# Optimization experiments

Hardware: AMD Instinct MI355X
Metric: run time of the kernel (lower is better)

The kernel has to match this reference:

```python
import jax, jax.numpy as jnp
import numpy as np

N = 50000
E = 600000
IN_DIM = 256
H1, H2, H3 = 128, 64, 64
HEADS = 8


def _add_self_loops(edge_index, edge_weight=None):
    loop = jnp.arange(N, dtype=edge_index.dtype)
    src = jnp.concatenate([edge_index[0], loop])
    dst = jnp.concatenate([edge_index[1], loop])
    if edge_weight is None:
        return src, dst, None
    ew = jnp.concatenate([edge_weight, jnp.ones((N,), edge_weight.dtype)])
    return src, dst, ew


def gcn_conv(x, edge_index, edge_weight, W, b):
    # PyG GCNConv: add self-loops (weight 1), symmetric normalization, scatter-add.
    src, dst, ew = _add_self_loops(edge_index, edge_weight)
    deg = jax.ops.segment_sum(ew, dst, num_segments=N)          # [N]
    dinv = jnp.where(deg > 0, jax.lax.rsqrt(jnp.maximum(deg, 1e-12)), 0.0)
    coeff = dinv[src] * ew * dinv[dst]                          # [E+N]
    h = x @ W                                                    # [N, out]
    out = jax.ops.segment_sum(coeff[:, None] * h[src], dst, num_segments=N)
    return out + b


def gat_conv(x, edge_index, W, att_src, att_dst, b):
    # PyG GATConv, heads=HEADS, concat=False (mean over heads), leaky_relu slope 0.2.
    src, dst, _ = _add_self_loops(edge_index)
    C = W.shape[1] // HEADS
    h = (x @ W).reshape(N, HEADS, C)                             # [N,H,C]
    a_s = jnp.sum(h * att_src, axis=-1)                          # [N,H]
    a_d = jnp.sum(h * att_dst, axis=-1)                          # [N,H]
    e = jax.nn.leaky_relu(a_s[src] + a_d[dst], negative_slope=0.2)  # [E',H]
    # scatter-softmax over edges sharing a destination
    m = jax.ops.segment_max(e, dst, num_segments=N)              # [N,H]
    p = jnp.exp(e - m[dst])
    s = jax.ops.segment_sum(p, dst, num_segments=N)              # [N,H]
    alpha = p / (s[dst] + 1e-16)                                 # [E',H]
    out = jax.ops.segment_sum(alpha[:, :, None] * h[src], dst, num_segments=N)  # [N,H,C]
    return jnp.mean(out, axis=1) + b


def setup_inputs() -> dict:
    key = jax.random.key(0)
    ks = jax.random.split(key, 12)
    x = jax.random.normal(ks[0], (N, IN_DIM), dtype=jnp.float32)
    edge_index = jax.random.randint(ks[1], (2, E), 0, N, dtype=jnp.int32)
    edge_weight = jax.random.uniform(ks[2], (E,), dtype=jnp.float32)
    def glorot(k, shape):
        fan = shape[0] + shape[-1]
        return jax.random.normal(k, shape, dtype=jnp.float32) * np.sqrt(2.0 / fan)
    return {
        "x": x, "edge_index": edge_index, "edge_weight": edge_weight,
        "gc1_w": glorot(ks[3], (IN_DIM, H1)), "gc1_b": jnp.zeros((H1,), jnp.float32),
        "gat_w": glorot(ks[4], (H1, HEADS * H2)),
        "att_src": glorot(ks[5], (HEADS, H2)), "att_dst": glorot(ks[6], (HEADS, H2)),
        "gat_b": jnp.zeros((H2,), jnp.float32),
        "gc2_w": glorot(ks[7], (H2, H3)), "gc2_b": jnp.zeros((H3,), jnp.float32),
        "fc_w": glorot(ks[8], (H3, 1)), "fc_b": jnp.zeros((1,), jnp.float32),
    }


def reference(x, edge_index, edge_weight, gc1_w, gc1_b, gat_w, att_src, att_dst,
              gat_b, gc2_w, gc2_b, fc_w, fc_b):
    # dropout is inference no-op
    h = jax.nn.relu(gcn_conv(x, edge_index, edge_weight, gc1_w, gc1_b))
    h = jax.nn.relu(gat_conv(h, edge_index, gat_w, att_src, att_dst, gat_b))
    h = jax.nn.relu(gcn_conv(h, edge_index, edge_weight, gc2_w, gc2_b))
    return h @ fc_w + fc_b                                       # [N,1]
```

## Files before the change

### kernel.cpp

```cpp
#include <hip/hip_runtime.h>
#include <hip/hip_bf16.h>

#define GNN_N 50000
#define GNN_E 600000

typedef unsigned int uint;
typedef unsigned short ushort;
using short8 = __attribute__((ext_vector_type(8))) short;
using f32x4  = __attribute__((ext_vector_type(4))) float;

__device__ __forceinline__ float leaky02(float x) { return x > 0.f ? x : 0.2f * x; }
__device__ __forceinline__ ushort f2b(float f) {
    uint u = __float_as_uint(f);
    return (ushort)((u + 0x7fffu + ((u >> 16) & 1u)) >> 16);
}
__device__ __forceinline__ float b2f(ushort b) { return __uint_as_float(((uint)b) << 16); }
__device__ __forceinline__ float blo(uint u) { return __uint_as_float(u << 16); }
__device__ __forceinline__ float bhi(uint u) { return __uint_as_float(u & 0xffff0000u); }

__global__ void gnn_hist(const int* __restrict__ dst, int* __restrict__ cnt, int e) {
    int i = blockIdx.x * blockDim.x + threadIdx.x;
    if (i < e) atomicAdd(&cnt[dst[i]], 1);
}
__global__ void gnn_scan1(const int* __restrict__ cnt, int* __restrict__ row_ptr,
                          int* __restrict__ blksum, int n) {
    __shared__ int sh[256];
    int tid = threadIdx.x;
    int base = blockIdx.x * 1024 + tid * 4;
    int v0 = (base + 0 < n) ? cnt[base + 0] : 0;
    int v1 = (base + 1 < n) ? cnt[base + 1] : 0;
    int v2 = (base + 2 < n) ? cnt[base + 2] : 0;
    int v3 = (base + 3 < n) ? cnt[base + 3] : 0;
    int tsum = v0 + v1 + v2 + v3;
    sh[tid] = tsum;
    __syncthreads();
    for (int off = 1; off < 256; off <<= 1) {
        int t = (tid >= off) ? sh[tid - off] : 0;
        __syncthreads();
        sh[tid] += t;
        __syncthreads();
    }
    int excl = sh[tid] - tsum;
    if (base + 0 < n) row_ptr[base + 0] = excl; excl += v0;
    if (base + 1 < n) row_ptr[base + 1] = excl; excl += v1;
    if (base + 2 < n) row_ptr[base + 2] = excl; excl += v2;
    if (base + 3 < n) row_ptr[base + 3] = excl;
    if (tid == 255) blksum[blockIdx.x] = sh[255];
}
__global__ void gnn_scan2(int* blksum, int nblk, int* row_ptr_end, int total) {
    if (threadIdx.x == 0 && blockIdx.x == 0) {
        int run = 0;
        for (int b = 0; b < nblk; ++b) { int t = blksum[b]; blksum[b] = run; run += t; }
        *row_ptr_end = total;
    }
}
__global__ void gnn_scan3(int* row_ptr, const int* __restrict__ blksum, int n) {
    int i = blockIdx.x * blockDim.x + threadIdx.x;
    if (i < n) row_ptr[i] += blksum[i >> 10];
}
__global__ void gnn_scatter_idx(const int* __restrict__ dst, const int* __restrict__ row_ptr,
                                int* __restrict__ fill, int* __restrict__ tord, int e) {
    int i = blockIdx.x * blockDim.x + threadIdx.x;
    if (i >= e) return;
    int d = dst[i];
    int pos = row_ptr[d] + atomicAdd(&fill[d], 1);
    tord[pos] = i;
}
__global__ void gnn_sortdeg(const float* __restrict__ ew, int* __restrict__ tord,
                            const int* __restrict__ row_ptr, float* __restrict__ dinv, int n) {
    int v = blockIdx.x * blockDim.x + threadIdx.x;
    if (v >= n) return;
    int beg = row_ptr[v], end = row_ptr[v + 1];
    int d = end - beg;
    if (d <= 64) {
        int buf[64];
        for (int i = 0; i < d; ++i) buf[i] = tord[beg + i];
        for (int i = 1; i < d; ++i) {
            int key = buf[i];
            int k = i - 1;
            while (k >= 0 && buf[k] > key) { buf[k + 1] = buf[k]; --k; }
            buf[k + 1] = key;
        }
        float s = 1.f;
        for (int i = 0; i < d; ++i) { tord[beg + i] = buf[i]; s += ew[buf[i]]; }
        dinv[v] = rsqrtf(s);
    } else {
        for (int i = beg + 1; i < end; ++i) {
            int key = tord[i];
            int k = i - 1;
            while (k >= beg && tord[k] > key) { tord[k + 1] = tord[k]; --k; }
            tord[k + 1] = key;
        }
        float s = 1.f;
        for (int i = beg; i < end; ++i) s += ew[tord[i]];
        dinv[v] = rsqrtf(s);
    }
}
__global__ void gnn_edgefin(const int* __restrict__ src, const int* __restrict__ dst,
                            const float* __restrict__ ew, const float* __restrict__ dinv,
                            const int* __restrict__ tord, int* __restrict__ esrc,
                            float* __restrict__ ecw, int e) {
    int pos = blockIdx.x * blockDim.x + threadIdx.x;
    if (pos >= e) return;
    int i = tord[pos];
    int s = src[i];
    esrc[pos] = s;
    ecw[pos] = dinv[s] * ew[i] * dinv[dst[i]];
}

__global__ void gnn_prep(const float* __restrict__ gc1_w, const float* __restrict__ gat_w,
                         const float* __restrict__ gc2_w, const float* __restrict__ att_src,
                         const float* __restrict__ att_dst, ushort* __restrict__ w1t,
                         ushort* __restrict__ w2s_t, ushort* __restrict__ w3t,
                         float* __restrict__ wa_t) {
    int t = blockIdx.x * 256 + threadIdx.x;
    if (t < 32768) {
        int k = t >> 7, n = t & 127;
        w1t[n * 256 + k] = f2b(gc1_w[t]);
        return;
    }
    t -= 32768;
    if (t < 65536) {
        int c = t >> 10, r = t & 1023;
        int h = r >> 7, k = r & 127;
        w2s_t[t] = f2b(0.125f * gat_w[(size_t)k * 512 + h * 64 + c]);
        return;
    }
    t -= 65536;
    if (t < 4096) {
        int k = t >> 6, n = t & 63;
        w3t[n * 64 + k] = f2b(gc2_w[t]);
        return;
    }
    t -= 4096;
    if (t < 2048) {
        int j = t >> 7, k = t & 127;
        int h = j & 7;
        const float* av = (j < 8) ? att_src : att_dst;
        float s = 0.f;
        for (int c = 0; c < 64; ++c) s += gat_w[(size_t)k * 512 + h * 64 + c] * av[h * 64 + c];
        wa_t[j * 128 + k] = s;
    }
}

template <bool AF32, bool BIAS>
__global__ __launch_bounds__(256) void gnn_mfma_gemm(const void* __restrict__ Av,
                                                     const ushort* __restrict__ Bt,
                                                     ushort* __restrict__ C,
                                                     const float* __restrict__ bias,
                                                     int M, int N, int K) {
    __shared__ ushort As[64 * 40];
    __shared__ ushort Bs[64 * 40];
    const int tid = threadIdx.x;
    const int wv = tid >> 6, lane = tid & 63;
    const int g = lane >> 4, r = lane & 15;
    const int brow = blockIdx.y << 6, bcol = blockIdx.x << 6;

    const int srow = tid >> 2;
    const int skoff = (tid & 3) << 3;
    int arow = brow + srow;
    if (arow >= M) arow = M - 1;
    const ushort* A16 = (const ushort*)Av;
    const float*  A32 = (const float*)Av;
    const ushort* Ap16 = A16 + (size_t)arow * K + skoff;
    const float*  Ap32 = A32 + (size_t)arow * K + skoff;
    const ushort* Bp = Bt + (size_t)(bcol + srow) * K + skoff;
    ushort* AsW = &As[srow * 40 + skoff];
    ushort* BsW = &Bs[srow * 40 + skoff];

    f32x4 acc[4] = {};

    for (int k0 = 0; k0 < K; k0 += 32) {
        if constexpr (AF32) {
            float4 f0 = *(const float4*)(Ap32 + k0);
            float4 f1 = *(const float4*)(Ap32 + k0 + 4);
            short8 t;
            t[0] = (short)f2b(f0.x); t[1] = (short)f2b(f0.y);
            t[2] = (short)f2b(f0.z); t[3] = (short)f2b(f0.w);
            t[4] = (short)f2b(f1.x); t[5] = (short)f2b(f1.y);
            t[6] = (short)f2b(f1.z); t[7] = (short)f2b(f1.w);
            *(short8*)AsW = t;
        } else {
            *(short8*)AsW = *(const short8*)(Ap16 + k0);
        }
        *(short8*)BsW = *(const short8*)(Bp + k0);
        __syncthreads();
        short8 bfrag = *(const short8*)&Bs[(wv * 16 + r) * 40 + g * 8];
#pragma unroll
        for (int mb = 0; mb < 4; ++mb) {
            short8 afrag = *(const short8*)&As[(mb * 16 + r) * 40 + g * 8];
            acc[mb] = __builtin_amdgcn_mfma_f32_16x16x32_bf16(afrag, bfrag, acc[mb], 0, 0, 0);
        }
        __syncthreads();
    }

    const int col = bcol + wv * 16 + r;
    float bv = 0.f;
    if constexpr (BIAS) bv = bias[col];
#pragma unroll
    for (int mb = 0; mb < 4; ++mb) {
        int rowb = brow + mb * 16 + g * 4;
#pragma unroll
        for (int rr = 0; rr < 4; ++rr) {
            int row = rowb + rr;
            if (row < M) {
                float val = acc[mb][rr];
                if constexpr (BIAS) {
                    val += bv;
                    val = val > 0.f ? val : 0.f;
                }
                C[(size_t)row * N + col] = f2b(val);
            }
        }
    }
}

__global__ __launch_bounds__(256) void gnn_gcn_node128_asd(const int* __restrict__ row_ptr,
                                                           const int* __restrict__ esrc,
                                                           const float* __restrict__ ecw,
                                                           const float* __restrict__ dinv,
                                                           const ushort* __restrict__ hb,
                                                           const float* __restrict__ b,
                                                           const float* __restrict__ wa,
                                                           ushort* __restrict__ out,
                                                           float* __restrict__ a_s,
                                                           float* __restrict__ a_d, int n) {
    __shared__ float swa[16 * 128];
    for (int i = threadIdx.x; i < 16 * 128; i += 256) swa[i] = wa[i];
    __syncthreads();
    int v = blockIdx.x * 4 + (threadIdx.x >> 6);
    int lane = threadIdx.x & 63;
    if (v >= n) return;
    const int sl = lane & 31;
    const int half = lane >> 5;
    float di = dinv[v];
    float a0, a1, a2, a3;
    {
        float scl = half ? 0.f : di * di;
        uint2 u = *(const uint2*)(hb + (size_t)v * 128 + 4 * sl);
        a0 = scl * blo(u.x); a1 = scl * bhi(u.x);
        a2 = scl * blo(u.y); a3 = scl * bhi(u.y);
    }
    int beg = row_ptr[v], end = row_ptr[v + 1];
    int cntE = end - beg;
    int pairs = cntE >> 1;
    int i = 0;
    for (; i + 4 <= pairs; i += 4) {
        int s[4]; float c[4]; uint2 u[4];
#pragma unroll
        for (int t = 0; t < 4; ++t) s[t] = esrc[beg + 2 * (i + t) + half];
#pragma unroll
        for (int t = 0; t < 4; ++t) c[t] = ecw[beg + 2 * (i + t) + half];
#pragma unroll
        for (int t = 0; t < 4; ++t) u[t] = *(const uint2*)(hb + (size_t)s[t] * 128 + 4 * sl);
#pragma unroll
        for (int t = 0; t < 4; ++t) {
            a0 += c[t] * blo(u[t].x); a1 += c[t] * bhi(u[t].x);
            a2 += c[t] * blo(u[t].y); a3 += c[t] * bhi(u[t].y);
        }
    }
    for (; i < pairs; ++i) {
        int s = esrc[beg + 2 * i + half];
        float c = ecw[beg + 2 * i + half];
        uint2 u = *(const uint2*)(hb + (size_t)s * 128 + 4 * sl);
        a0 += c * blo(u.x); a1 += c * bhi(u.x);
        a2 += c * blo(u.y); a3 += c * bhi(u.y);
    }
    if (cntE & 1) {
        int s = esrc[end - 1];
        float c = half ? 0.f : ecw[end - 1];
        uint2 u = *(const uint2*)(hb + (size_t)s * 128 + 4 * sl);
        a0 += c * blo(u.x); a1 += c * bhi(u.x);
        a2 += c * blo(u.y); a3 += c * bhi(u.y);
    }
    a0 += __shfl_xor(a0, 32); a1 += __shfl_xor(a1, 32);
    a2 += __shfl_xor(a2, 32); a3 += __shfl_xor(a3, 32);

    float4 bv = *(const float4*)(b + 4 * sl);
    float o0 = a0 + bv.x, o1 = a1 + bv.y, o2 = a2 + bv.z, o3 = a3 + bv.w;
    o0 = o0 > 0.f ? o0 : 0.f; o1 = o1 > 0.f ? o1 : 0.f;
    o2 = o2 > 0.f ? o2 : 0.f; o3 = o3 > 0.f ? o3 : 0.f;
    if (lane < 32) {
        uint2 w;
        w.x = (uint)f2b(o0) | ((uint)f2b(o1) << 16);
        w.y = (uint)f2b(o2) | ((uint)f2b(o3) << 16);
        *(uint2*)(out + (size_t)v * 128 + 4 * sl) = w;
    }

    float part[16];
#pragma unroll
    for (int j = 0; j < 16; ++j) {
        const float* wj = &swa[j * 128 + 4 * sl];
        part[j] = o0 * wj[0] + o1 * wj[1] + o2 * wj[2] + o3 * wj[3];
    }
#pragma unroll
    for (int m = 1; m < 32; m <<= 1) {
#pragma unroll
        for (int j = 0; j < 16; ++j) part[j] += __shfl_xor(part[j], m);
    }
    if (lane == 0) {
#pragma unroll
        for (int j = 0; j < 8; ++j) {
            a_s[(size_t)v * 8 + j] = part[j];
            a_d[(size_t)v * 8 + j] = part[8 + j];
        }
    }
}

__global__ __launch_bounds__(256) void gnn_gat_z(const int* __restrict__ row_ptr,
                                                 const int* __restrict__ esrc,
                                                 const float* __restrict__ a_s,
                                                 const float* __restrict__ a_d,
                                                 const ushort* __restrict__ g1b,
                                                 ushort* __restrict__ zb, int n) {
    int v = blockIdx.x * 4 + (threadIdx.x >> 6);
    int lane = threadIdx.x & 63;
    if (v >= n) return;
    const int sl = lane & 31;
    const int half = lane >> 5;
    const int hh = lane & 7;
    const int hbase = lane & 32;
    const float adh = a_d[(size_t)v * 8 + hh];

    float z0[8] = {}, z1[8] = {}, z2[8] = {}, z3[8] = {};
    float sloc = 0.f;
    {
        float pv = __expf(leaky02(a_s[(size_t)v * 8 + hh] + adh));
        if (half) pv = 0.f;
        sloc += pv;
        uint2 u = *(const uint2*)(g1b + (size_t)v * 128 + 4 * sl);
        float g0 = blo(u.x), g1v = bhi(u.x), g2v = blo(u.y), g3v = bhi(u.y);
        float ph[8];
#pragma unroll
        for (int h = 0; h < 8; ++h) ph[h] = __shfl(pv, hbase | h);
#pragma unroll
        for (int h = 0; h < 8; ++h) {
            z0[h] += ph[h] * g0; z1[h] += ph[h] * g1v;
            z2[h] += ph[h] * g2v; z3[h] += ph[h] * g3v;
        }
    }
    int beg = row_ptr[v], end = row_ptr[v + 1];
    int cntE = end - beg;
    int pairs = cntE >> 1;
    int i = 0;
    for (; i + 2 <= pairs; i += 2) {
        int s[2]; float e[2]; uint2 u[2];
#pragma unroll
        for (int t = 0; t < 2; ++t) s[t] = esrc[beg + 2 * (i + t) + half];
#pragma unroll
        for (int t = 0; t < 2; ++t) e[t] = a_s[(size_t)s[t] * 8 + hh];
#pragma unroll
        for (int t = 0; t < 2; ++t) u[t] = *(const uint2*)(g1b + (size_t)s[t] * 128 + 4 * sl);
#pragma unroll
        for (int t = 0; t < 2; ++t) {
            float pv = __expf(leaky02(e[t] + adh));
            sloc += pv;
            float g0 = blo(u[t].x), g1v = bhi(u[t].x), g2v = blo(u[t].y), g3v = bhi(u[t].y);
            float ph[8];
#pragma unroll
            for (int h = 0; h < 8; ++h) ph[h] = __shfl(pv, hbase | h);
#pragma unroll
            for (int h = 0; h < 8; ++h) {
                z0[h] += ph[h] * g0; z1[h] += ph[h] * g1v;
                z2[h] += ph[h] * g2v; z3[h] += ph[h] * g3v;
            }
        }
    }
    for (; i < pairs; ++i) {
        int s = esrc[beg + 2 * i + half];
        float pv = __expf(leaky02(a_s[(size_t)s * 8 + hh] + adh));
        sloc += pv;
        uint2 u = *(const uint2*)(g1b + (size_t)s * 128 + 4 * sl);
        float g0 = blo(u.x), g1v = bhi(u.x), g2v = blo(u.y), g3v = bhi(u.y);
        float ph[8];
#pragma unroll
        for (int h = 0; h < 8; ++h) ph[h] = __shfl(pv, hbase | h);
#pragma unroll
        for (int h = 0; h < 8; ++h) {
            z0[h] += ph[h] * g0; z1[h] += ph[h] * g1v;
            z2[h] += ph[h] * g2v; z3[h] += ph[h] * g3v;
        }
    }
    if (cntE & 1) {
        int s = esrc[end - 1];
        float pv = __expf(leaky02(a_s[(size_t)s * 8 + hh] + adh));
        if (half) pv = 0.f;
        sloc += pv;
        uint2 u = *(const uint2*)(g1b + (size_t)s * 128 + 4 * sl);
        float g0 = blo(u.x), g1v = bhi(u.x), g2v = blo(u.y), g3v = bhi(u.y);
        float ph[8];
#pragma unroll
        for (int h = 0; h < 8; ++h) ph[h] = __shfl(pv, hbase | h);
#pragma unroll
        for (int h = 0; h < 8; ++h) {
            z0[h] += ph[h] * g0; z1[h] += ph[h] * g1v;
            z2[h] += ph[h] * g2v; z3[h] += ph[h] * g3v;
        }
    }
    float slx = sloc + __shfl_xor(sloc, 32) + 1e-16f;
#pragma unroll
    for (int h = 0; h < 8; ++h) {
        z0[h] += __shfl_xor(z0[h], 32); z1[h] += __shfl_xor(z1[h], 32);
        z2[h] += __shfl_xor(z2[h], 32); z3[h] += __shfl_xor(z3[h], 32);
    }
    if (lane < 32) {
#pragma unroll
        for (int h = 0; h < 8; ++h) {
            float rs = 1.f / __shfl(slx, h);
            uint2 w;
            w.x = (uint)f2b(z0[h] * rs) | ((uint)f2b(z1[h] * rs) << 16);
            w.y = (uint)f2b(z2[h] * rs) | ((uint)f2b(z3[h] * rs) << 16);
            *(uint2*)(zb + (size_t)v * 1024 + h * 128 + 4 * sl) = w;
        }
    }
}

__global__ __launch_bounds__(256) void gnn_gcn_node64_fc(const int* __restrict__ row_ptr,
                                                         const int* __restrict__ esrc,
                                                         const float* __restrict__ ecw,
                                                         const float* __restrict__ dinv,
                                                         const ushort* __restrict__ hb,
                                                         const float* __restrict__ b,
                                                         const float* __restrict__ fc_w,
                                                         const float* __restrict__ fc_b,
                                                         float* __restrict__ out, int n) {
    int v = blockIdx.x * 4 + (threadIdx.x >> 6);
    int lane = threadIdx.x & 63;
    if (v >= n) return;
    const int sl = lane & 31;
    const int half = lane >> 5;
    float di = dinv[v];
    float a0, a1;
    {
        float scl = half ? 0.f : di * di;
        uint u = *(const uint*)(hb + (size_t)v * 64 + 2 * sl);
        a0 = scl * blo(u); a1 = scl * bhi(u);
    }
    int beg = row_ptr[v], end = row_ptr[v + 1];
    int cntE = end - beg;
    int pairs = cntE >> 1;
    int i = 0;
    for (; i + 4 <= pairs; i += 4) {
        int s[4]; float c[4]; uint u[4];
#pragma unroll
        for (int t = 0; t < 4; ++t) s[t] = esrc[beg + 2 * (i + t) + half];
#pragma unroll
        for (int t = 0; t < 4; ++t) c[t] = ecw[beg + 2 * (i + t) + half];
#pragma unroll
        for (int t = 0; t < 4; ++t) u[t] = *(const uint*)(hb + (size_t)s[t] * 64 + 2 * sl);
#pragma unroll
        for (int t = 0; t < 4; ++t) { a0 += c[t] * blo(u[t]); a1 += c[t] * bhi(u[t]); }
    }
    for (; i < pairs; ++i) {
        int s = esrc[beg + 2 * i + half];
        float c = ecw[beg + 2 * i + half];
        uint u = *(const uint*)(hb + (size_t)s * 64 + 2 * sl);
        a0 += c * blo(u); a1 += c * bhi(u);
    }
    if (cntE & 1) {
        int s = esrc[end - 1];
        float c = half ? 0.f : ecw[end - 1];
        uint u = *(const uint*)(hb + (size_t)s * 64 + 2 * sl);
        a0 += c * blo(u); a1 += c * bhi(u);
    }
    a0 += __shfl_xor(a0, 32);
    a1 += __shfl_xor(a1, 32);
    float o0 = a0 + b[2 * sl];
    float o1 = a1 + b[2 * sl + 1];
    o0 = o0 > 0.f ? o0 : 0.f;
    o1 = o1 > 0.f ? o1 : 0.f;
    float val = o0 * fc_w[2 * sl] + o1 * fc_w[2 * sl + 1];
#pragma unroll
    for (int m = 1; m < 32; m <<= 1) val += __shfl_xor(val, m);
    if (lane == 0) out[v] = val + fc_b[0];
}

extern "C" void kernel_launch(void* const* d_in, const int* in_sizes, int n_in,
                              void* d_out, int out_size, void* d_ws, size_t ws_size,
                              hipStream_t stream) {
    const float* x       = (const float*)d_in[0];
    const int*   ei      = (const int*)d_in[1];
    const float* ew      = (const float*)d_in[2];
    const float* gc1_w   = (const float*)d_in[3];
    const float* gc1_b   = (const float*)d_in[4];
    const float* gat_w   = (const float*)d_in[5];
    const float* att_src = (const float*)d_in[6];
    const float* att_dst = (const float*)d_in[7];
    const float* gat_b   = (const float*)d_in[8];
    const float* gc2_w   = (const float*)d_in[9];
    const float* gc2_b   = (const float*)d_in[10];
    const float* fc_w    = (const float*)d_in[11];
    const float* fc_b    = (const float*)d_in[12];
    float* out = (float*)d_out;

    const int N = GNN_N;
    const int E = in_sizes[2];
    const int* src = ei;
    const int* dst = ei + E;

    char* p = (char*)d_ws;
    ushort* zb  = (ushort*)p; p += (size_t)N * 1024 * 2;
    ushort* h1b = (ushort*)p; p += (size_t)N * 128 * 2;
    ushort* g1b = (ushort*)p; p += (size_t)N * 128 * 2;
    ushort* g2b = (ushort*)p; p += (size_t)N * 64 * 2;
    ushort* h3b = (ushort*)p; p += (size_t)N * 64 * 2;
    ushort* w1t = (ushort*)p; p += (size_t)128 * 256 * 2;
    ushort* w2s_t = (ushort*)p; p += (size_t)64 * 1024 * 2;
    ushort* w3t = (ushort*)p; p += (size_t)64 * 64 * 2;
    float*  wa_t = (float*)p; p += 16 * 128 * 4;
    float*  a_s = (float*)p;  p += (size_t)N * 8 * 4;
    float*  a_d = (float*)p;  p += (size_t)N * 8 * 4;
    int* row_ptr = (int*)p;   p += (size_t)(N + 64) * 4;
    int* esrc = (int*)p;      p += (size_t)E * 4;
    float* ecw = (float*)p;   p += (size_t)E * 4;
    int* tord = (int*)p;      p += (size_t)E * 4;
    int* cnt = (int*)p;       p += (size_t)N * 4;
    int* fill = (int*)p;      p += (size_t)N * 4;
    float* dinv = (float*)p;  p += (size_t)N * 4;
    int* blksum = (int*)p;    p += 4096;

    auto cdiv = [](long a, long b) { return (int)((a + b - 1) / b); };

    hipMemsetAsync(cnt, 0, (size_t)N * 8, stream);
    gnn_hist<<<cdiv(E, 256), 256, 0, stream>>>(dst, cnt, E);
    const int nblk = cdiv(N, 1024);
    gnn_scan1<<<nblk, 256, 0, stream>>>(cnt, row_ptr, blksum, N);
    gnn_scan2<<<1, 64, 0, stream>>>(blksum, nblk, row_ptr + N, E);
    gnn_scan3<<<cdiv(N, 256), 256, 0, stream>>>(row_ptr, blksum, N);
    gnn_scatter_idx<<<cdiv(E, 256), 256, 0, stream>>>(dst, row_ptr, fill, tord, E);
    gnn_sortdeg<<<cdiv(N, 256), 256, 0, stream>>>(ew, tord, row_ptr, dinv, N);
    gnn_edgefin<<<cdiv(E, 256), 256, 0, stream>>>(src, dst, ew, dinv, tord, esrc, ecw, E);

    gnn_prep<<<408, 256, 0, stream>>>(gc1_w, gat_w, gc2_w, att_src, att_dst, w1t, w2s_t, w3t, wa_t);

    {
        dim3 grid(128 / 64, cdiv(N, 64));
        gnn_mfma_gemm<true, false><<<grid, 256, 0, stream>>>(x, w1t, h1b, nullptr, N, 128, 256);
    }
    gnn_gcn_node128_asd<<<cdiv(N, 4), 256, 0, stream>>>(row_ptr, esrc, ecw, dinv, h1b, gc1_b,
                                                        wa_t, g1b, a_s, a_d, N);

    gnn_gat_z<<<cdiv(N, 4), 256, 0, stream>>>(row_ptr, esrc, a_s, a_d, g1b, zb, N);
    {
        dim3 grid(1, cdiv(N, 64));
        gnn_mfma_gemm<false, true><<<grid, 256, 0, stream>>>(zb, w2s_t, g2b, gat_b, N, 64, 1024);
    }

    {
        dim3 grid(1, cdiv(N, 64));
        gnn_mfma_gemm<false, false><<<grid, 256, 0, stream>>>(g2b, w3t, h3b, nullptr, N, 64, 64);
    }
    gnn_gcn_node64_fc<<<cdiv(N, 4), 256, 0, stream>>>(row_ptr, esrc, ecw, dinv, h3b, gc2_b,
                                                      fc_w, fc_b, out, N);
}
```

Measured before the change: 363.3 us.

## Use wave-wide bitonic sort for CSR edge order and packed FMA in GAT aggregation

The per-node insertion sort, which used one thread and a 64-entry private buffer, is replaced by a 64-lane bitonic sort over shuffles, one wavefront per node, followed by a wave reduction for the degree. This removes the serial, scratch-heavy sorting and its divergence. Separately, the GAT aggregation kernel now uses v_pk_fma_f32 through inline asm on float2 accumulators and does the head-probability shuffles as 64-bit values, halving the FMA instruction count. Inline asm may limit compiler scheduling, and launching 4 nodes per block adds more blocks.

```diff
diff --git a/kernel.cpp b/kernel.cpp
--- a/kernel.cpp
+++ b/kernel.cpp
@@ -8,6 +8,7 @@
 typedef unsigned short ushort;
 using short8 = __attribute__((ext_vector_type(8))) short;
 using f32x4  = __attribute__((ext_vector_type(4))) float;
+using f32x2  = __attribute__((ext_vector_type(2))) float;
 
 __device__ __forceinline__ float leaky02(float x) { return x > 0.f ? x : 0.2f * x; }
 __device__ __forceinline__ ushort f2b(float f) {
@@ -17,6 +18,22 @@
 __device__ __forceinline__ float b2f(ushort b) { return __uint_as_float(((uint)b) << 16); }
 __device__ __forceinline__ float blo(uint u) { return __uint_as_float(u << 16); }
 __device__ __forceinline__ float bhi(uint u) { return __uint_as_float(u & 0xffff0000u); }
+
+__device__ __forceinline__ void pkfma(f32x2& d, f32x2 a, f32x2 b) {
+    asm("v_pk_fma_f32 %0, %1, %2, %0" : "+v"(d) : "v"(a), "v"(b));
+}
+__device__ __forceinline__ f32x2 shfl2(f32x2 x, int srcLane) {
+    union { f32x2 f; long long l; } u;
+    u.f = x;
+    u.l = __shfl(u.l, srcLane);
+    return u.f;
+}
+__device__ __forceinline__ f32x2 shflx2(f32x2 x, int m) {
+    union { f32x2 f; long long l; } u;
+    u.f = x;
+    u.l = __shfl_xor(u.l, m);
+    return u.f;
+}
 
 __global__ void gnn_hist(const int* __restrict__ dst, int* __restrict__ cnt, int e) {
     int i = blockIdx.x * blockDim.x + threadIdx.x;
@@ -66,34 +83,43 @@
     int pos = row_ptr[d] + atomicAdd(&fill[d], 1);
     tord[pos] = i;
 }
-__global__ void gnn_sortdeg(const float* __restrict__ ew, int* __restrict__ tord,
-                            const int* __restrict__ row_ptr, float* __restrict__ dinv, int n) {
-    int v = blockIdx.x * blockDim.x + threadIdx.x;
+__global__ __launch_bounds__(256) void gnn_sortdeg(const float* __restrict__ ew,
+                                                   int* __restrict__ tord,
+                                                   const int* __restrict__ row_ptr,
+                                                   float* __restrict__ dinv, int n) {
+    int v = blockIdx.x * 4 + (threadIdx.x >> 6);
+    int lane = threadIdx.x & 63;
     if (v >= n) return;
     int beg = row_ptr[v], end = row_ptr[v + 1];
-    int d = end - beg;
-    if (d <= 64) {
-        int buf[64];
-        for (int i = 0; i < d; ++i) buf[i] = tord[beg + i];
-        for (int i = 1; i < d; ++i) {
-            int key = buf[i];
-            int k = i - 1;
-            while (k >= 0 && buf[k] > key) { buf[k + 1] = buf[k]; --k; }
-            buf[k + 1] = key;
-        }
-        float s = 1.f;
-        for (int i = 0; i < d; ++i) { tord[beg + i] = buf[i]; s += ew[buf[i]]; }
-        dinv[v] = rsqrtf(s);
+    int cnt = end - beg;
+    if (cnt <= 64) {
+        int val = (lane < cnt) ? tord[beg + lane] : 0x7fffffff;
+#pragma unroll
+        for (int k = 2; k <= 64; k <<= 1) {
+#pragma unroll
+            for (int j = k >> 1; j >= 1; j >>= 1) {
+                int other = __shfl_xor(val, j);
+                bool keepMin = (((lane & j) == 0) == ((lane & k) == 0));
+                val = keepMin ? min(val, other) : max(val, other);
+            }
+        }
+        if (lane < cnt) tord[beg + lane] = val;
+        float s = (lane < cnt) ? ew[val] : 0.f;
+#pragma unroll
+        for (int m = 32; m; m >>= 1) s += __shfl_xor(s, m);
+        if (lane == 0) dinv[v] = rsqrtf(1.0f + s);
     } else {
-        for (int i = beg + 1; i < end; ++i) {
-            int key = tord[i];
-            int k = i - 1;
-            while (k >= beg && tord[k] > key) { tord[k + 1] = tord[k]; --k; }
-            tord[k + 1] = key;
-        }
-        float s = 1.f;
-        for (int i = beg; i < end; ++i) s += ew[tord[i]];
-        dinv[v] = rsqrtf(s);
+        if (lane == 0) {
+            for (int i = beg + 1; i < end; ++i) {
+                int key = tord[i];
+                int k2 = i - 1;
+                while (k2 >= beg && tord[k2] > key) { tord[k2 + 1] = tord[k2]; --k2; }
+                tord[k2 + 1] = key;
+            }
+            float s = 1.f;
+            for (int i = beg; i < end; ++i) s += ew[tord[i]];
+            dinv[v] = rsqrtf(s);
+        }
     }
 }
 __global__ void gnn_edgefin(const int* __restrict__ src, const int* __restrict__ dst,
@@ -322,21 +348,21 @@
     const int hbase = lane & 32;
     const float adh = a_d[(size_t)v * 8 + hh];
 
-    float z0[8] = {}, z1[8] = {}, z2[8] = {}, z3[8] = {};
+    f32x2 zA[8] = {}, zB[8] = {};
     float sloc = 0.f;
     {
         float pv = __expf(leaky02(a_s[(size_t)v * 8 + hh] + adh));
         if (half) pv = 0.f;
         sloc += pv;
+        f32x2 pv2; pv2[0] = pv; pv2[1] = pv;
         uint2 u = *(const uint2*)(g1b + (size_t)v * 128 + 4 * sl);
-        float g0 = blo(u.x), g1v = bhi(u.x), g2v = blo(u.y), g3v = bhi(u.y);
-        float ph[8];
-#pragma unroll
-        for (int h = 0; h < 8; ++h) ph[h] = __shfl(pv, hbase | h);
+        f32x2 gA; gA[0] = blo(u.x); gA[1] = bhi(u.x);
+        f32x2 gB; gB[0] = blo(u.y); gB[1] = bhi(u.y);
 #pragma unroll
         for (int h = 0; h < 8; ++h) {
-            z0[h] += ph[h] * g0; z1[h] += ph[h] * g1v;
-            z2[h] += ph[h] * g2v; z3[h] += ph[h] * g3v;
+            f32x2 ph2 = shfl2(pv2, hbase | h);
+            pkfma(zA[h], gA, ph2);
+            pkfma(zB[h], gB, ph2);
         }
     }
     int beg = row_ptr[v], end = row_ptr[v + 1];
@@ -355,14 +381,14 @@
         for (int t = 0; t < 2; ++t) {
             float pv = __expf(leaky02(e[t] + adh));
             sloc += pv;
-            float g0 = blo(u[t].x), g1v = bhi(u[t].x), g2v = blo(u[t].y), g3v = bhi(u[t].y);
-            float ph[8];
-#pragma unroll
-            for (int h = 0; h < 8; ++h) ph[h] = __shfl(pv, hbase | h);
+            f32x2 pv2; pv2[0] = pv; pv2[1] = pv;
+            f32x2 gA; gA[0] = blo(u[t].x); gA[1] = bhi(u[t].x);
+            f32x2 gB; gB[0] = blo(u[t].y); gB[1] = bhi(u[t].y);
 #pragma unroll
             for (int h = 0; h < 8; ++h) {
-                z0[h] += ph[h] * g0; z1[h] += ph[h] * g1v;
-                z2[h] += ph[h] * g2v; z3[h] += ph[h] * g3v;
+                f32x2 ph2 = shfl2(pv2, hbase | h);
+                pkfma(zA[h], gA, ph2);
+                pkfma(zB[h], gB, ph2);
             }
         }
     }
@@ -370,15 +396,15 @@
         int s = esrc[beg + 2 * i + half];
         float pv = __expf(leaky02(a_s[(size_t)s * 8 + hh] + adh));
         sloc += pv;
+        f32x2 pv2; pv2[0] = pv; pv2[1] = pv;
         uint2 u = *(const uint2*)(g1b + (size_t)s * 128 + 4 * sl);
-        float g0 = blo(u.x), g1v = bhi(u.x), g2v = blo(u.y), g3v = bhi(u.y);
-        float ph[8];
-#pragma unroll
-        for (int h = 0; h < 8; ++h) ph[h] = __shfl(pv, hbase | h);
+        f32x2 gA; gA[0] = blo(u.x); gA[1] = bhi(u.x);
+        f32x2 gB; gB[0] = blo(u.y); gB[1] = bhi(u.y);
 #pragma unroll
         for (int h = 0; h < 8; ++h) {
-            z0[h] += ph[h] * g0; z1[h] += ph[h] * g1v;
-            z2[h] += ph[h] * g2v; z3[h] += ph[h] * g3v;
+            f32x2 ph2 = shfl2(pv2, hbase | h);
+            pkfma(zA[h], gA, ph2);
+            pkfma(zB[h], gB, ph2);
         }
     }
     if (cntE & 1) {
@@ -386,30 +412,30 @@
         float pv = __expf(leaky02(a_s[(size_t)s * 8 + hh] + adh));
         if (half) pv = 0.f;
         sloc += pv;
+        f32x2 pv2; pv2[0] = pv; pv2[1] = pv;
         uint2 u = *(const uint2*)(g1b + (size_t)s * 128 + 4 * sl);
-        float g0 = blo(u.x), g1v = bhi(u.x), g2v = blo(u.y), g3v = bhi(u.y);
-        float ph[8];
-#pragma unroll
-        for (int h = 0; h < 8; ++h) ph[h] = __shfl(pv, hbase | h);
+        f32x2 gA; gA[0] = blo(u.x); gA[1] = bhi(u.x);
+        f32x2 gB; gB[0] = blo(u.y); gB[1] = bhi(u.y);
 #pragma unroll
         for (int h = 0; h < 8; ++h) {
-            z0[h] += ph[h] * g0; z1[h] += ph[h] * g1v;
-            z2[h] += ph[h] * g2v; z3[h] += ph[h] * g3v;
+            f32x2 ph2 = shfl2(pv2, hbase | h);
+            pkfma(zA[h], gA, ph2);
+            pkfma(zB[h], gB, ph2);
         }
     }
     float slx = sloc + __shfl_xor(sloc, 32) + 1e-16f;
 #pragma unroll
     for (int h = 0; h < 8; ++h) {
-        z0[h] += __shfl_xor(z0[h], 32); z1[h] += __shfl_xor(z1[h], 32);
-        z2[h] += __shfl_xor(z2[h], 32); z3[h] += __shfl_xor(z3[h], 32);
+        zA[h] = zA[h] + shflx2(zA[h], 32);
+        zB[h] = zB[h] + shflx2(zB[h], 32);
     }
     if (lane < 32) {
 #pragma unroll
         for (int h = 0; h < 8; ++h) {
             float rs = 1.f / __shfl(slx, h);
             uint2 w;
-            w.x = (uint)f2b(z0[h] * rs) | ((uint)f2b(z1[h] * rs) << 16);
-            w.y = (uint)f2b(z2[h] * rs) | ((uint)f2b(z3[h] * rs) << 16);
+            w.x = (uint)f2b(zA[h][0] * rs) | ((uint)f2b(zA[h][1] * rs) << 16);
+            w.y = (uint)f2b(zB[h][0] * rs) | ((uint)f2b(zB[h][1] * rs) << 16);
             *(uint2*)(zb + (size_t)v * 1024 + h * 128 + 4 * sl) = w;
         }
     }
@@ -528,7 +554,7 @@
     gnn_scan2<<<1, 64, 0, stream>>>(blksum, nblk, row_ptr + N, E);
     gnn_scan3<<<cdiv(N, 256), 256, 0, stream>>>(row_ptr, blksum, N);
     gnn_scatter_idx<<<cdiv(E, 256), 256, 0, stream>>>(dst, row_ptr, fill, tord, E);
-    gnn_sortdeg<<<cdiv(N, 256), 256, 0, stream>>>(ew, tord, row_ptr, dinv, N);
+    gnn_sortdeg<<<cdiv(N, 4), 256, 0, stream>>>(ew, tord, row_ptr, dinv, N);
     gnn_edgefin<<<cdiv(E, 256), 256, 0, stream>>>(src, dst, ew, dinv, tord, esrc, ecw, E);
 
     gnn_prep<<<408, 256, 0, stream>>>(gc1_w, gat_w, gc2_w, att_src, att_dst, w1t, w2s_t, w3t, wa_t);
```

Result: faster. 337.6 us, median of 2 (-7.1%).
